# Performance work log

Hardware: AMD Instinct MI355X
Metric: run time of the kernel (lower is better)

The kernel has to match this reference:

```python
import jax, jax.numpy as jnp
import numpy as np

D = 1024          # model dim
W = 4             # window size
H = 16
HD = D // H       # head dim
LN_EPS = 1e-5


def setup_inputs() -> dict:
    key = jax.random.key(0)
    ks = jax.random.split(key, 8)
    B, N = 4, 8192
    s = 1.0 / np.sqrt(D)
    return {
        "x": jax.random.normal(ks[0], (B, N, D), dtype=jnp.float32),
        # nn.MultiheadAttention packed in-projection: [3D, D] weight, [3D] bias
        "in_proj_w": jax.random.uniform(ks[1], (3 * D, D), minval=-s, maxval=s, dtype=jnp.float32),
        "in_proj_b": jax.random.uniform(ks[2], (3 * D,), minval=-s, maxval=s, dtype=jnp.float32),
        "out_proj_w": jax.random.uniform(ks[3], (D, D), minval=-s, maxval=s, dtype=jnp.float32),
        "out_proj_b": jnp.zeros((D,), dtype=jnp.float32),
        "ln_gamma": jnp.ones((D,), dtype=jnp.float32),
        "ln_beta": jnp.zeros((D,), dtype=jnp.float32),
        # gate is a learned scalar (init zero in torch); use nonzero so attn path is exercised
        "gate": jnp.full((1,), 0.5, dtype=jnp.float32),
    }


def _local_attn_gate(x, in_proj_w, in_proj_b, out_proj_w, out_proj_b, ln_gamma, ln_beta, gate):
    B, N, _ = x.shape
    pad = (-N) % W
    xp = jnp.pad(x, ((0, 0), (0, pad), (0, 0))) if pad else x
    Np = xp.shape[1]
    nW = Np // W

    # packed qkv projection: [B, Np, 3D]
    qkv = xp @ in_proj_w.T + in_proj_b
    q, k, v = jnp.split(qkv, 3, axis=-1)

    def to_win(t):  # [B, Np, D] -> [B, nW, W, H, HD]
        return t.reshape(B, nW, W, H, HD)

    q, k, v = to_win(q), to_win(k), to_win(v)

    scale = 1.0 / np.sqrt(HD)
    # per-window attention scores: [B, nW, H, W, W]
    scores = jnp.einsum("bnqhd,bnkhd->bnhqk", q, k) * scale
    attn = jax.nn.softmax(scores, axis=-1)
    out = jnp.einsum("bnhqk,bnkhd->bnqhd", attn, v).reshape(B, Np, D)
    out = out @ out_proj_w.T + out_proj_b
    out = out[:, :N, :]

    y = x + gate[0] * out
    mu = jnp.mean(y, axis=-1, keepdims=True)
    var = jnp.mean(jnp.square(y - mu), axis=-1, keepdims=True)
    return (y - mu) * jax.lax.rsqrt(var + LN_EPS) * ln_gamma + ln_beta


def reference(x, in_proj_w, in_proj_b, out_proj_w, out_proj_b, ln_gamma, ln_beta, gate):
    return _local_attn_gate(x, in_proj_w, in_proj_b, out_proj_w, out_proj_b, ln_gamma, ln_beta, gate)
```

## Files before the change

### kernel.cpp

```cpp
#include <hip/hip_runtime.h>
#include <stdint.h>

typedef __attribute__((ext_vector_type(8))) short short8;
typedef __attribute__((ext_vector_type(4))) float floatx4;

__device__ __forceinline__ float bf2f(uint16_t u) {
  union { uint32_t u; float f; } c; c.u = (uint32_t)u << 16; return c.f;
}
__device__ __forceinline__ uint16_t f2bf(float f) {
  union { float f; uint32_t u; } c; c.f = f;
  return (uint16_t)((c.u + 0x7fffu + ((c.u >> 16) & 1u)) >> 16);
}
__device__ __forceinline__ void gload_lds16(const void* g, void* l) {
  __builtin_amdgcn_global_load_lds(
      (const __attribute__((address_space(1))) uint32_t*)g,
      (__attribute__((address_space(3))) uint32_t*)l, 16, 0, 0);
}
__device__ __forceinline__ short8 cvt8(const float* src, size_t u) {
  const floatx4* p = (const floatx4*)src + u * 2;
  floatx4 a = p[0], b = p[1];
  short8 o;
  o[0] = (short)f2bf(a[0]); o[1] = (short)f2bf(a[1]);
  o[2] = (short)f2bf(a[2]); o[3] = (short)f2bf(a[3]);
  o[4] = (short)f2bf(b[0]); o[5] = (short)f2bf(b[1]);
  o[6] = (short)f2bf(b[2]); o[7] = (short)f2bf(b[3]);
  return o;
}

__global__ void k_cvt_all(const float* __restrict__ x, const float* __restrict__ wi,
                          const float* __restrict__ wo, const float* __restrict__ bi,
                          uint16_t* __restrict__ xb, uint16_t* __restrict__ wib,
                          uint16_t* __restrict__ wob, float* __restrict__ bip) {
  const int NX = 4194304, NWI = 393216, NWO = 131072, NB = 384;
  int i = blockIdx.x * 256 + threadIdx.x;
  if (i < NX) {
    *((short8*)xb + i) = cvt8(x, i);
  } else if (i < NX + NWI) {
    int j = i - NX;
    int row = j >> 7, cu = j & 127;
    int h = (row & 1023) >> 6, t = row >> 10, d = row & 63;
    int nrow = h * 192 + t * 64 + d;
    *((short8*)wib + (size_t)nrow * 128 + cu) = cvt8(wi, j);
  } else if (i < NX + NWI + NWO) {
    int j = i - NX - NWI;
    *((short8*)wob + j) = cvt8(wo, j);
  } else if (i < NX + NWI + NWO + NB) {
    int j = i - NX - NWI - NWO;
    int b0 = j * 8;
    int h = (b0 & 1023) >> 6, t = b0 >> 10, d = b0 & 63;
    int dst = h * 192 + t * 64 + d;
#pragma unroll
    for (int e = 0; e < 8; e++) bip[dst + e] = bi[b0 + e];
  }
}

__device__ __forceinline__ void decode_bid(int bid, int nwg, int ncols,
                                           int* mblk, int* nblk) {
  const int q = nwg >> 3;
  const int wg = (bid & 7) * q + (bid >> 3);
  *nblk = wg % ncols;
  *mblk = wg / ncols;
}

__global__ __launch_bounds__(256, 3) void k_gemm_qkv_attn(
    const uint16_t* __restrict__ A, const uint16_t* __restrict__ Wt,
    const float* __restrict__ bias, uint16_t* __restrict__ attn_o,
    int K, int nwg) {
  __shared__ __align__(16) unsigned char lds_raw[51200];
  uint16_t* lds_a  = (uint16_t*)lds_raw;
  uint16_t* lds_b  = (uint16_t*)(lds_raw + 16384);
  uint16_t* lds_ep = (uint16_t*)lds_raw;

  const int t = threadIdx.x;
  const int wave = t >> 6, lane = t & 63;
  const int wr = wave >> 1, wc = wave & 1;
  int mblk, nblk;
  decode_bid(blockIdx.x, nwg, 16, &mblk, &nblk);
  const int m0 = mblk * 128, n0 = nblk * 192;

  const char* gA = (const char*)(A + (size_t)(m0 + (t >> 2)) * K) + (t & 3) * 16;
  const char* gB = (const char*)(Wt + (size_t)(n0 + (t >> 2)) * K) + (t & 3) * 16;
  const size_t rs64 = (size_t)64 * K * 2;
  const int ksub = lane >> 4, rrow = lane & 15;
  const int nT = K / 32;

  floatx4 acc[4][6];
#pragma unroll
  for (int i = 0; i < 4; i++)
#pragma unroll
    for (int j = 0; j < 6; j++) acc[i][j] = (floatx4){0.f, 0.f, 0.f, 0.f};

  auto stage = [&](int tile) {
    char* lA = (char*)lds_a + (tile & 1) * 8192 + wave * 1024;
    char* lB = (char*)lds_b + (tile & 1) * 12288 + wave * 1024;
    const char* ga = gA + (size_t)tile * 64;
    const char* gb = gB + (size_t)tile * 64;
    gload_lds16(ga, lA);
    gload_lds16(ga + rs64, lA + 4096);
    gload_lds16(gb, lB);
    gload_lds16(gb + rs64, lB + 4096);
    gload_lds16(gb + 2 * rs64, lB + 8192);
  };

  stage(0);
  __syncthreads();
  for (int tt = 0; tt < nT; ++tt) {
    if (tt + 1 < nT) stage(tt + 1);
    const short8* pa = (const short8*)(lds_a + (tt & 1) * 4096);
    const short8* pb = (const short8*)(lds_b + (tt & 1) * 6144);
    short8 af[4], bfr[6];
#pragma unroll
    for (int i = 0; i < 4; i++)
      af[i] = pa[(wr * 64 + i * 16 + rrow) * 4 + ksub];
#pragma unroll
    for (int j = 0; j < 6; j++)
      bfr[j] = pb[(wc * 96 + j * 16 + rrow) * 4 + ksub];
#pragma unroll
    for (int i = 0; i < 4; i++)
#pragma unroll
      for (int j = 0; j < 6; j++)
        acc[i][j] = __builtin_amdgcn_mfma_f32_16x16x32_bf16(af[i], bfr[j], acc[i][j], 0, 0, 0);
    __syncthreads();
  }

  const int cq = lane >> 4, cr = lane & 15;
#pragma unroll
  for (int j = 0; j < 6; j++) {
    int col = wc * 96 + j * 16 + cr;
    float bv = bias[n0 + col];
#pragma unroll
    for (int i = 0; i < 4; i++) {
      int row = wr * 64 + i * 16 + cq * 4;
#pragma unroll
      for (int rg = 0; rg < 4; rg++)
        lds_ep[(size_t)(row + rg) * 200 + col] = f2bf(acc[i][j][rg] + bv);
    }
  }
  __syncthreads();

  const int h = nblk;
  const int g8 = lane >> 3, s8 = lane & 7;
  const int r0 = (wave * 8 + g8) * 4;
  float q[4][8], k[4][8], v[4][8];
#pragma unroll
  for (int i = 0; i < 4; i++) {
    const uint16_t* rp = lds_ep + (size_t)(r0 + i) * 200;
    short8 qv = *(const short8*)(rp + s8 * 8);
    short8 kv = *(const short8*)(rp + 64 + s8 * 8);
    short8 vv = *(const short8*)(rp + 128 + s8 * 8);
#pragma unroll
    for (int d = 0; d < 8; d++) {
      q[i][d] = bf2f((uint16_t)qv[d]);
      k[i][d] = bf2f((uint16_t)kv[d]);
      v[i][d] = bf2f((uint16_t)vv[d]);
    }
  }
  float s[4][4];
#pragma unroll
  for (int qi = 0; qi < 4; qi++)
#pragma unroll
    for (int ki = 0; ki < 4; ki++) {
      float a = 0.f;
#pragma unroll
      for (int d = 0; d < 8; d++) a = fmaf(q[qi][d], k[ki][d], a);
      s[qi][ki] = a;
    }
#pragma unroll
  for (int off = 1; off <= 4; off <<= 1)
#pragma unroll
    for (int qi = 0; qi < 4; qi++)
#pragma unroll
      for (int ki = 0; ki < 4; ki++)
        s[qi][ki] += __shfl_xor(s[qi][ki], off, 64);

#pragma unroll
  for (int qi = 0; qi < 4; qi++) {
    float a0 = s[qi][0] * 0.125f, a1 = s[qi][1] * 0.125f;
    float a2 = s[qi][2] * 0.125f, a3 = s[qi][3] * 0.125f;
    float m = fmaxf(fmaxf(a0, a1), fmaxf(a2, a3));
    float e0 = __expf(a0 - m), e1 = __expf(a1 - m);
    float e2 = __expf(a2 - m), e3 = __expf(a3 - m);
    float inv = 1.f / (e0 + e1 + e2 + e3);
    short8 ov;
#pragma unroll
    for (int d = 0; d < 8; d++) {
      float o = (e0 * v[0][d] + e1 * v[1][d] + e2 * v[2][d] + e3 * v[3][d]) * inv;
      ov[d] = (short)f2bf(o);
    }
    *(short8*)(attn_o + (size_t)(m0 + r0 + qi) * 1024 + h * 64 + s8 * 8) = ov;
  }
}

__device__ __forceinline__ void gemm_main(
    const uint16_t* __restrict__ A, const uint16_t* __restrict__ Wt, int K,
    uint16_t* lds_a, uint16_t* lds_b, int m0, int n0, floatx4 acc[4][4]) {
  const int t = threadIdx.x;
  const int wave = t >> 6, lane = t & 63;
  const int wr = wave >> 1, wc = wave & 1;
  const int r = t >> 2;
  const int cb = (t & 3) * 16;
  const char* gA = (const char*)(A + (size_t)(m0 + r) * K) + cb;
  const char* gB = (const char*)(Wt + (size_t)(n0 + r) * K) + cb;
  const size_t rowskip = (size_t)64 * K * 2;
  const int ksub = lane >> 4, rrow = lane & 15;
  const int nT = K / 32;

  {
    char* lA = (char*)lds_a + wave * 1024;
    char* lB = (char*)lds_b + wave * 1024;
    gload_lds16(gA, lA);
    gload_lds16(gA + rowskip, lA + 4096);
    gload_lds16(gB, lB);
    gload_lds16(gB + rowskip, lB + 4096);
    gA += 64; gB += 64;
  }
  __syncthreads();

  int c = 0;
  for (int tt = 0; tt < nT; ++tt) {
    if (tt + 1 < nT) {
      char* lA = (char*)lds_a + (c ^ 1) * 8192 + wave * 1024;
      char* lB = (char*)lds_b + (c ^ 1) * 8192 + wave * 1024;
      gload_lds16(gA, lA);
      gload_lds16(gA + rowskip, lA + 4096);
      gload_lds16(gB, lB);
      gload_lds16(gB + rowskip, lB + 4096);
      gA += 64; gB += 64;
    }
    const short8* pa = (const short8*)(lds_a + c * 4096);
    const short8* pb = (const short8*)(lds_b + c * 4096);
    short8 af[4], bfr[4];
#pragma unroll
    for (int i = 0; i < 4; i++)
      af[i] = pa[(wr * 64 + i * 16 + rrow) * 4 + ksub];
#pragma unroll
    for (int j = 0; j < 4; j++)
      bfr[j] = pb[(wc * 64 + j * 16 + rrow) * 4 + ksub];
#pragma unroll
    for (int i = 0; i < 4; i++)
#pragma unroll
      for (int j = 0; j < 4; j++)
        acc[i][j] = __builtin_amdgcn_mfma_f32_16x16x32_bf16(af[i], bfr[j], acc[i][j], 0, 0, 0);
    __syncthreads();
    c ^= 1;
  }
}

__global__ __launch_bounds__(256, 2) void k_gemm_out(
    const uint16_t* __restrict__ A, const uint16_t* __restrict__ Wt,
    const float* __restrict__ bias, const uint16_t* __restrict__ xres_bf,
    const float* __restrict__ gate, uint16_t* __restrict__ Y,
    int K, int N, int nwg, int ncols) {
  __shared__ __align__(16) uint16_t lds_a[2 * 128 * 32];
  __shared__ __align__(16) uint16_t lds_b[2 * 128 * 32];
  floatx4 acc[4][4];
#pragma unroll
  for (int i = 0; i < 4; i++)
#pragma unroll
    for (int j = 0; j < 4; j++) acc[i][j] = (floatx4){0.f, 0.f, 0.f, 0.f};
  int mblk, nblk;
  decode_bid(blockIdx.x, nwg, ncols, &mblk, &nblk);
  const int m0 = mblk * 128, n0 = nblk * 128;
  gemm_main(A, Wt, K, lds_a, lds_b, m0, n0, acc);
  const float g = gate[0];
  const int wave = threadIdx.x >> 6, lane = threadIdx.x & 63;
  const int wr = wave >> 1, wc = wave & 1;
  const int cq = lane >> 4, cr = lane & 15;
#pragma unroll
  for (int j = 0; j < 4; j++) {
    int col = n0 + wc * 64 + j * 16 + cr;
    float bv = bias[col];
#pragma unroll
    for (int i = 0; i < 4; i++) {
      int row = m0 + wr * 64 + i * 16 + cq * 4;
#pragma unroll
      for (int rg = 0; rg < 4; rg++) {
        float o = acc[i][j][rg] + bv;
        float xv = bf2f(xres_bf[(size_t)(row + rg) * N + col]);
        Y[(size_t)(row + rg) * N + col] = f2bf(xv + g * o);
      }
    }
  }
}

__global__ __launch_bounds__(256) void k_ln(
    const uint16_t* __restrict__ y, const float* __restrict__ gamma,
    const float* __restrict__ beta, float* __restrict__ out) {
  const int wave = threadIdx.x >> 6, lane = threadIdx.x & 63;
  const size_t row = (size_t)blockIdx.x * 4 + wave;
  const uint16_t* py = y + row * 1024 + lane * 16;
  short8 v0 = *(const short8*)py;
  short8 v1 = *(const short8*)(py + 8);
  float f[16];
#pragma unroll
  for (int j = 0; j < 8; j++) {
    f[j] = bf2f((uint16_t)v0[j]);
    f[8 + j] = bf2f((uint16_t)v1[j]);
  }
  float sum = 0.f, sq = 0.f;
#pragma unroll
  for (int j = 0; j < 16; j++) { sum += f[j]; sq += f[j] * f[j]; }
#pragma unroll
  for (int off = 32; off; off >>= 1) {
    sum += __shfl_xor(sum, off, 64);
    sq  += __shfl_xor(sq,  off, 64);
  }
  const float mu = sum * (1.f / 1024.f);
  const float var = sq * (1.f / 1024.f) - mu * mu;
  const float inv = rsqrtf(var + 1e-5f);
  const int c0 = lane * 16;
  float* po = out + row * 1024 + lane * 16;
#pragma unroll
  for (int c = 0; c < 4; c++) {
    floatx4 o;
#pragma unroll
    for (int e = 0; e < 4; e++) {
      int j = c * 4 + e;
      o[e] = (f[j] - mu) * inv * gamma[c0 + j] + beta[c0 + j];
    }
    *(floatx4*)(po + c * 4) = o;
  }
}

extern "C" void kernel_launch(void* const* d_in, const int* in_sizes, int n_in,
                              void* d_out, int out_size, void* d_ws, size_t ws_size,
                              hipStream_t stream) {
  const float* x     = (const float*)d_in[0];
  const float* w_in  = (const float*)d_in[1];
  const float* b_in  = (const float*)d_in[2];
  const float* w_out = (const float*)d_in[3];
  const float* b_out = (const float*)d_in[4];
  const float* gamma = (const float*)d_in[5];
  const float* beta  = (const float*)d_in[6];
  const float* gate  = (const float*)d_in[7];
  float* out = (float*)d_out;

  const int M = 32768;
  char* ws = (char*)d_ws;
  uint16_t* w_in_bf  = (uint16_t*)ws;
  uint16_t* w_out_bf = (uint16_t*)(ws + 6291456);
  float*    b_in_p   = (float*)(ws + 8388608);
  uint16_t* x_bf     = (uint16_t*)(ws + 8404992);
  uint16_t* attn_bf  = (uint16_t*)(ws + 8404992 + 67108864);
  uint16_t* y_bf     = (uint16_t*)(ws + 8404992 + 67108864 + 67108864);

  k_cvt_all<<<18434, 256, 0, stream>>>(x, w_in, w_out, b_in,
                                       x_bf, w_in_bf, w_out_bf, b_in_p);

  const int nwg1 = (M / 128) * 16;
  const int nwg2 = (M / 128) * (1024 / 128);
  k_gemm_qkv_attn<<<nwg1, 256, 0, stream>>>(
      x_bf, w_in_bf, b_in_p, attn_bf, 1024, nwg1);
  k_gemm_out<<<nwg2, 256, 0, stream>>>(
      attn_bf, w_out_bf, b_out, x_bf, gate, y_bf, 1024, 1024, nwg2, 1024 / 128);
  k_ln<<<M / 4, 256, 0, stream>>>(y_bf, gamma, beta, out);
}
```

Measured before the change: 443.0 us.

## Enlarge output-projection GEMM tile to 256x128 with inlined pipelined main loop

The output-projection GEMM now uses 256x128 block tiles instead of 128x128, so each wave computes an 8x4 grid of MFMA fragments. Doubling the M tile halves the number of workgroups and cuts how often weight tiles are reloaded per output element. The LDS staging layout is redone to match, and the shared gemm_main helper is inlined into the kernel. In exchange the kernel needs more accumulator registers and more LDS, which may lower occupancy against the requested 2 blocks per CU.

After: 452.0 us. 2.0% more time.

```diff
diff --git a/kernel.cpp b/kernel.cpp
--- a/kernel.cpp
+++ b/kernel.cpp
@@ -191,88 +191,81 @@
   }
 }
 
-__device__ __forceinline__ void gemm_main(
-    const uint16_t* __restrict__ A, const uint16_t* __restrict__ Wt, int K,
-    uint16_t* lds_a, uint16_t* lds_b, int m0, int n0, floatx4 acc[4][4]) {
-  const int t = threadIdx.x;
-  const int wave = t >> 6, lane = t & 63;
-  const int wr = wave >> 1, wc = wave & 1;
-  const int r = t >> 2;
-  const int cb = (t & 3) * 16;
-  const char* gA = (const char*)(A + (size_t)(m0 + r) * K) + cb;
-  const char* gB = (const char*)(Wt + (size_t)(n0 + r) * K) + cb;
-  const size_t rowskip = (size_t)64 * K * 2;
-  const int ksub = lane >> 4, rrow = lane & 15;
-  const int nT = K / 32;
-
-  {
-    char* lA = (char*)lds_a + wave * 1024;
-    char* lB = (char*)lds_b + wave * 1024;
-    gload_lds16(gA, lA);
-    gload_lds16(gA + rowskip, lA + 4096);
-    gload_lds16(gB, lB);
-    gload_lds16(gB + rowskip, lB + 4096);
-    gA += 64; gB += 64;
-  }
-  __syncthreads();
-
-  int c = 0;
-  for (int tt = 0; tt < nT; ++tt) {
-    if (tt + 1 < nT) {
-      char* lA = (char*)lds_a + (c ^ 1) * 8192 + wave * 1024;
-      char* lB = (char*)lds_b + (c ^ 1) * 8192 + wave * 1024;
-      gload_lds16(gA, lA);
-      gload_lds16(gA + rowskip, lA + 4096);
-      gload_lds16(gB, lB);
-      gload_lds16(gB + rowskip, lB + 4096);
-      gA += 64; gB += 64;
-    }
-    const short8* pa = (const short8*)(lds_a + c * 4096);
-    const short8* pb = (const short8*)(lds_b + c * 4096);
-    short8 af[4], bfr[4];
-#pragma unroll
-    for (int i = 0; i < 4; i++)
-      af[i] = pa[(wr * 64 + i * 16 + rrow) * 4 + ksub];
-#pragma unroll
-    for (int j = 0; j < 4; j++)
-      bfr[j] = pb[(wc * 64 + j * 16 + rrow) * 4 + ksub];
-#pragma unroll
-    for (int i = 0; i < 4; i++)
-#pragma unroll
-      for (int j = 0; j < 4; j++)
-        acc[i][j] = __builtin_amdgcn_mfma_f32_16x16x32_bf16(af[i], bfr[j], acc[i][j], 0, 0, 0);
-    __syncthreads();
-    c ^= 1;
-  }
-}
-
 __global__ __launch_bounds__(256, 2) void k_gemm_out(
     const uint16_t* __restrict__ A, const uint16_t* __restrict__ Wt,
     const float* __restrict__ bias, const uint16_t* __restrict__ xres_bf,
     const float* __restrict__ gate, uint16_t* __restrict__ Y,
-    int K, int N, int nwg, int ncols) {
-  __shared__ __align__(16) uint16_t lds_a[2 * 128 * 32];
-  __shared__ __align__(16) uint16_t lds_b[2 * 128 * 32];
-  floatx4 acc[4][4];
-#pragma unroll
-  for (int i = 0; i < 4; i++)
+    int K, int N, int nwg) {
+  __shared__ __align__(16) unsigned char lds_raw[49152];
+  uint16_t* lds_a = (uint16_t*)lds_raw;
+  uint16_t* lds_b = (uint16_t*)(lds_raw + 32768);
+
+  const int t = threadIdx.x;
+  const int wave = t >> 6, lane = t & 63;
+  const int wr = wave >> 1, wc = wave & 1;
+  int mblk, nblk;
+  decode_bid(blockIdx.x, nwg, 8, &mblk, &nblk);
+  const int m0 = mblk * 256, n0 = nblk * 128;
+
+  const int srow = lane >> 2, scol = (lane & 3) * 16;
+  const int a0 = wave * 4, b0 = wave * 2;
+  const char* pA0 = (const char*)(A + (size_t)(m0 + (a0 + 0) * 16 + srow) * K) + scol;
+  const char* pA1 = (const char*)(A + (size_t)(m0 + (a0 + 1) * 16 + srow) * K) + scol;
+  const char* pA2 = (const char*)(A + (size_t)(m0 + (a0 + 2) * 16 + srow) * K) + scol;
+  const char* pA3 = (const char*)(A + (size_t)(m0 + (a0 + 3) * 16 + srow) * K) + scol;
+  const char* pB0 = (const char*)(Wt + (size_t)(n0 + (b0 + 0) * 16 + srow) * K) + scol;
+  const char* pB1 = (const char*)(Wt + (size_t)(n0 + (b0 + 1) * 16 + srow) * K) + scol;
+  const int ksub = lane >> 4, rrow = lane & 15;
+  const int nT = K / 32;
+
+  floatx4 acc[8][4];
+#pragma unroll
+  for (int i = 0; i < 8; i++)
 #pragma unroll
     for (int j = 0; j < 4; j++) acc[i][j] = (floatx4){0.f, 0.f, 0.f, 0.f};
-  int mblk, nblk;
-  decode_bid(blockIdx.x, nwg, ncols, &mblk, &nblk);
-  const int m0 = mblk * 128, n0 = nblk * 128;
-  gemm_main(A, Wt, K, lds_a, lds_b, m0, n0, acc);
+
+  auto stage = [&](int tile) {
+    char* bufA = (char*)lds_a + (tile & 1) * 16384;
+    char* bufB = (char*)lds_b + (tile & 1) * 8192;
+    const size_t ko = (size_t)tile * 64;
+    gload_lds16(pA0 + ko, bufA + (a0 + 0) * 1024);
+    gload_lds16(pA1 + ko, bufA + (a0 + 1) * 1024);
+    gload_lds16(pA2 + ko, bufA + (a0 + 2) * 1024);
+    gload_lds16(pA3 + ko, bufA + (a0 + 3) * 1024);
+    gload_lds16(pB0 + ko, bufB + (b0 + 0) * 1024);
+    gload_lds16(pB1 + ko, bufB + (b0 + 1) * 1024);
+  };
+
+  stage(0);
+  __syncthreads();
+  for (int tt = 0; tt < nT; ++tt) {
+    if (tt + 1 < nT) stage(tt + 1);
+    const short8* pa = (const short8*)(lds_a + (tt & 1) * 8192);
+    const short8* pb = (const short8*)(lds_b + (tt & 1) * 4096);
+    short8 af[8], bfr[4];
+#pragma unroll
+    for (int i = 0; i < 8; i++)
+      af[i] = pa[(wr * 128 + i * 16 + rrow) * 4 + ksub];
+#pragma unroll
+    for (int j = 0; j < 4; j++)
+      bfr[j] = pb[(wc * 64 + j * 16 + rrow) * 4 + ksub];
+#pragma unroll
+    for (int i = 0; i < 8; i++)
+#pragma unroll
+      for (int j = 0; j < 4; j++)
+        acc[i][j] = __builtin_amdgcn_mfma_f32_16x16x32_bf16(af[i], bfr[j], acc[i][j], 0, 0, 0);
+    __syncthreads();
+  }
+
   const float g = gate[0];
-  const int wave = threadIdx.x >> 6, lane = threadIdx.x & 63;
-  const int wr = wave >> 1, wc = wave & 1;
   const int cq = lane >> 4, cr = lane & 15;
 #pragma unroll
   for (int j = 0; j < 4; j++) {
     int col = n0 + wc * 64 + j * 16 + cr;
     float bv = bias[col];
 #pragma unroll
-    for (int i = 0; i < 4; i++) {
-      int row = m0 + wr * 64 + i * 16 + cq * 4;
+    for (int i = 0; i < 8; i++) {
+      int row = m0 + wr * 128 + i * 16 + cq * 4;
 #pragma unroll
       for (int rg = 0; rg < 4; rg++) {
         float o = acc[i][j][rg] + bv;
@@ -348,10 +341,10 @@
                                        x_bf, w_in_bf, w_out_bf, b_in_p);
 
   const int nwg1 = (M / 128) * 16;
-  const int nwg2 = (M / 128) * (1024 / 128);
+  const int nwg2 = (M / 256) * (1024 / 128);
   k_gemm_qkv_attn<<<nwg1, 256, 0, stream>>>(
       x_bf, w_in_bf, b_in_p, attn_bf, 1024, nwg1);
   k_gemm_out<<<nwg2, 256, 0, stream>>>(
-      attn_bf, w_out_bf, b_out, x_bf, gate, y_bf, 1024, 1024, nwg2, 1024 / 128);
+      attn_bf, w_out_bf, b_out, x_bf, gate, y_bf, 1024, 1024, nwg2);
   k_ln<<<M / 4, 256, 0, stream>>>(y_bf, gamma, beta, out);
 }
```

## Triple-buffer QKV GEMM LDS loads with vmcnt-based waits and MFMA priority

Applied to the files above, without the earlier changes.

Moves the QKV projection GEMM main loop from double to triple buffering in LDS. Tile t+2 is prefetched while tile t is computed, using s_waitcnt vmcnt(5) plus a raw barrier in place of a full __syncthreads after every tile. MFMA sections are wrapped in s_setprio to favour math issue. This costs more LDS (60KB), so launch bounds drop from 3 to 2 workgroups per CU, lowering occupancy in exchange for deeper load latency hiding.

Result: slower. 455.2 us (+2.7%).

```diff
diff --git a/kernel.cpp b/kernel.cpp
--- a/kernel.cpp
+++ b/kernel.cpp
@@ -62,13 +62,13 @@
   *mblk = wg / ncols;
 }
 
-__global__ __launch_bounds__(256, 3) void k_gemm_qkv_attn(
+__global__ __launch_bounds__(256, 2) void k_gemm_qkv_attn(
     const uint16_t* __restrict__ A, const uint16_t* __restrict__ Wt,
     const float* __restrict__ bias, uint16_t* __restrict__ attn_o,
     int K, int nwg) {
-  __shared__ __align__(16) unsigned char lds_raw[51200];
+  __shared__ __align__(16) unsigned char lds_raw[61440];
   uint16_t* lds_a  = (uint16_t*)lds_raw;
-  uint16_t* lds_b  = (uint16_t*)(lds_raw + 16384);
+  uint16_t* lds_b  = (uint16_t*)(lds_raw + 24576);
   uint16_t* lds_ep = (uint16_t*)lds_raw;
 
   const int t = threadIdx.x;
@@ -90,9 +90,9 @@
 #pragma unroll
     for (int j = 0; j < 6; j++) acc[i][j] = (floatx4){0.f, 0.f, 0.f, 0.f};
 
-  auto stage = [&](int tile) {
-    char* lA = (char*)lds_a + (tile & 1) * 8192 + wave * 1024;
-    char* lB = (char*)lds_b + (tile & 1) * 12288 + wave * 1024;
+  auto stage = [&](int tile, int buf) {
+    char* lA = (char*)lds_a + buf * 8192 + wave * 1024;
+    char* lB = (char*)lds_b + buf * 12288 + wave * 1024;
     const char* ga = gA + (size_t)tile * 64;
     const char* gb = gB + (size_t)tile * 64;
     gload_lds16(ga, lA);
@@ -101,13 +101,9 @@
     gload_lds16(gb + rs64, lB + 4096);
     gload_lds16(gb + 2 * rs64, lB + 8192);
   };
-
-  stage(0);
-  __syncthreads();
-  for (int tt = 0; tt < nT; ++tt) {
-    if (tt + 1 < nT) stage(tt + 1);
-    const short8* pa = (const short8*)(lds_a + (tt & 1) * 4096);
-    const short8* pb = (const short8*)(lds_b + (tt & 1) * 6144);
+  auto compute = [&](int buf) {
+    const short8* pa = (const short8*)(lds_a + buf * 4096);
+    const short8* pb = (const short8*)(lds_b + buf * 6144);
     short8 af[4], bfr[6];
 #pragma unroll
     for (int i = 0; i < 4; i++)
@@ -115,13 +111,31 @@
 #pragma unroll
     for (int j = 0; j < 6; j++)
       bfr[j] = pb[(wc * 96 + j * 16 + rrow) * 4 + ksub];
+    __builtin_amdgcn_s_setprio(1);
 #pragma unroll
     for (int i = 0; i < 4; i++)
 #pragma unroll
       for (int j = 0; j < 6; j++)
         acc[i][j] = __builtin_amdgcn_mfma_f32_16x16x32_bf16(af[i], bfr[j], acc[i][j], 0, 0, 0);
-    __syncthreads();
-  }
+    __builtin_amdgcn_s_setprio(0);
+  };
+
+  stage(0, 0);
+  stage(1, 1);
+  int cc = 0;
+  int cs = 2;
+  for (int tt = 0; tt < nT - 1; ++tt) {
+    asm volatile("s_waitcnt vmcnt(5)" ::: "memory");
+    __builtin_amdgcn_s_barrier();
+    if (tt + 2 < nT) stage(tt + 2, cs);
+    compute(cc);
+    cc = (cc == 2) ? 0 : cc + 1;
+    cs = (cs == 2) ? 0 : cs + 1;
+  }
+  asm volatile("s_waitcnt vmcnt(0)" ::: "memory");
+  __builtin_amdgcn_s_barrier();
+  compute(cc);
+  __syncthreads();
 
   const int cq = lane >> 4, cr = lane & 15;
 #pragma unroll
```
